# Performance work log

Hardware: AMD Instinct MI355X
Metric: run time of the kernel (lower is better)

## Reference

```python
import jax, jax.numpy as jnp
import numpy as np

POOL_SIZE = 100
TOP_K = 5
EPS = 1e-12

def l2_normalize(x, axis):
    # matches module: x * rsqrt(max(sum(x^2), eps))
    sq = jnp.sum(x * x, axis=axis, keepdims=True)
    return x * jax.lax.rsqrt(jnp.maximum(sq, EPS))

def setup_inputs() -> dict:
    key = jax.random.key(0)
    k1, k2 = jax.random.split(key)
    x_embed = jax.random.normal(k1, (256, 512, 768), dtype=jnp.float32)
    # prompt_key init 'uniform' -> U(-1, 1)
    prompt_key = jax.random.uniform(k2, (POOL_SIZE, 768), dtype=jnp.float32, minval=-1.0, maxval=1.0)
    return {"x_embed": x_embed, "prompt_key": prompt_key}

def reference(x_embed, prompt_key):
    B = x_embed.shape[0]
    # embedding_key == 'cls' with cls_features=None -> max over sequence dim
    x_embed_mean = jnp.max(x_embed, axis=1)                      # [B, D]
    prompt_norm = l2_normalize(prompt_key, axis=1)               # [P, D]
    x_embed_norm = l2_normalize(x_embed_mean, axis=1)            # [B, D]
    similarity = jnp.matmul(x_embed_norm, prompt_norm.T)         # [B, P]
    _, idx = jax.lax.top_k(similarity, TOP_K)                    # [B, K] (batchwise_prompt=False)
    selected_key = prompt_norm[idx]                              # [B, K, D] gather
    sim = selected_key * x_embed_norm[:, None, :]                # [B, K, D]
    reduce_sim = jnp.sum(sim) / B
    return similarity, selected_key, reduce_sim, idx
```

## Files before the change

kernel.cpp:

```cpp
#include <hip/hip_runtime.h>
#include <float.h>

#define B 256
#define S 512
#define D 768
#define P 100
#define K 5
#define SPLIT 4
#define SCHUNK (S / SPLIT)
#define D4 (D / 4)

#define PART_OFF 0
#define PN_OFF   (SPLIT * B * D)

#define SIM_OFF 0
#define SEL_OFF (B * P)
#define RS_OFF  (SEL_OFF + B * K * D)
#define IDX_OFF (RS_OFF + 1)

__device__ inline float4 fmax4(float4 a, float4 b) {
    return make_float4(fmaxf(a.x, b.x), fmaxf(a.y, b.y),
                       fmaxf(a.z, b.z), fmaxf(a.w, b.w));
}

__device__ inline float precise_rsqrt(float tot) {
    float x = fmaxf(tot, 1e-12f);
    float r = rsqrtf(x);
    r = r * (1.5f - 0.5f * x * r * r);
    return r;
}

__global__ __launch_bounds__(192) void k_stage1(const float* __restrict__ x,
                                                const float* __restrict__ pk,
                                                float* __restrict__ ws,
                                                float* __restrict__ out) {
    __shared__ float lds[3];
    const int blk = blockIdx.x;
    const int t = threadIdx.x;

    if (blk < B * SPLIT) {
        const int b  = blk >> 2;
        const int sp = blk & 3;
        const float4* src = (const float4*)(x + (size_t)b * S * D)
                            + (size_t)(sp * SCHUNK) * D4 + t;
        float4 m0 = make_float4(-FLT_MAX, -FLT_MAX, -FLT_MAX, -FLT_MAX);
        float4 m1 = m0, m2 = m0, m3 = m0;
        for (int s = 0; s < SCHUNK; s += 4) {
            float4 a0 = src[(size_t)(s + 0) * D4];
            float4 a1 = src[(size_t)(s + 1) * D4];
            float4 a2 = src[(size_t)(s + 2) * D4];
            float4 a3 = src[(size_t)(s + 3) * D4];
            m0 = fmax4(m0, a0);
            m1 = fmax4(m1, a1);
            m2 = fmax4(m2, a2);
            m3 = fmax4(m3, a3);
        }
        float4 m = fmax4(fmax4(m0, m1), fmax4(m2, m3));
        ((float4*)(ws + PART_OFF))[(size_t)(sp * B + b) * D4 + t] = m;
    } else {
        const int p = blk - B * SPLIT;
        float4 v = ((const float4*)pk)[(size_t)p * D4 + t];
        float sq = v.x * v.x + v.y * v.y + v.z * v.z + v.w * v.w;
        for (int off = 32; off; off >>= 1) sq += __shfl_down(sq, off);
        const int lane = t & 63, w = t >> 6;
        if (lane == 0) lds[w] = sq;
        __syncthreads();
        float tot = lds[0] + lds[1] + lds[2];
        float r = precise_rsqrt(tot);
        ((float4*)(ws + PN_OFF))[(size_t)p * D4 + t] =
            make_float4(v.x * r, v.y * r, v.z * r, v.w * r);
        if (p == 0 && t == 0) out[RS_OFF] = 0.0f;
    }
}

__global__ __launch_bounds__(256) void k_fused(const float* __restrict__ ws,
                                               float* __restrict__ out) {
    __shared__ float xs[D];
    __shared__ float simbuf[P];
    __shared__ float lds[4];
    __shared__ float topv[K];
    __shared__ int   topi[K];
    const int b = blockIdx.x, t = threadIdx.x;
    const int w = t >> 6, lane = t & 63;

    float4 m = make_float4(0.f, 0.f, 0.f, 0.f);
    float sq = 0.f;
    if (t < D4) {
        const float4* part = (const float4*)(ws + PART_OFF);
        m = part[(size_t)b * D4 + t];
        #pragma unroll
        for (int sp = 1; sp < SPLIT; ++sp)
            m = fmax4(m, part[(size_t)(sp * B + b) * D4 + t]);
        sq = m.x * m.x + m.y * m.y + m.z * m.z + m.w * m.w;
    }
    for (int off = 32; off; off >>= 1) sq += __shfl_down(sq, off);
    if (lane == 0) lds[w] = sq;
    __syncthreads();
    float tot = lds[0] + lds[1] + lds[2] + lds[3];
    float r = precise_rsqrt(tot);
    if (t < D4)
        ((float4*)xs)[t] = make_float4(m.x * r, m.y * r, m.z * r, m.w * r);
    __syncthreads();

    const float* pn = ws + PN_OFF;
    for (int j = 0; j < 25; ++j) {
        const int p = w + 4 * j;
        float acc = 0.f;
        #pragma unroll
        for (int jj = 0; jj < 12; ++jj) {
            const int d = lane + 64 * jj;
            acc += pn[(size_t)p * D + d] * xs[d];
        }
        for (int off = 32; off; off >>= 1) acc += __shfl_down(acc, off);
        if (lane == 0) {
            simbuf[p] = acc;
            out[SIM_OFF + (size_t)b * P + p] = acc;
        }
    }
    __syncthreads();

    if (w == 0) {
        float v0 = (lane < P) ? simbuf[lane] : -FLT_MAX;
        int   i0 = lane;
        int   i1 = lane + 64;
        float v1 = (i1 < P) ? simbuf[i1] : -FLT_MAX;
        for (int k = 0; k < K; ++k) {
            float bv; int bi;
            if (v0 > v1 || (v0 == v1 && i0 < i1)) { bv = v0; bi = i0; }
            else                                  { bv = v1; bi = i1; }
            for (int off = 32; off; off >>= 1) {
                float ov = __shfl_xor(bv, off);
                int   oi = __shfl_xor(bi, off);
                if (ov > bv || (ov == bv && oi < bi)) { bv = ov; bi = oi; }
            }
            if (lane == 0) { topv[k] = bv; topi[k] = bi; }
            if (bi == i0) v0 = -FLT_MAX;
            else if (bi == i1) v1 = -FLT_MAX;
        }
    }
    __syncthreads();

    if (t < K) out[IDX_OFF + (size_t)b * K + t] = (float)topi[t];

    if (t == 0) {
        float s = topv[0] + topv[1] + topv[2] + topv[3] + topv[4];
        atomicAdd(out + RS_OFF, s * (1.0f / (float)B));
    }

    const float4* pn4 = (const float4*)pn;
    float4* sel4 = (float4*)(out + SEL_OFF) + (size_t)b * (K * D4);
    for (int i = t; i < K * D4; i += 256) {
        const int k = i / D4;
        const int e = i - k * D4;
        sel4[i] = pn4[(size_t)topi[k] * D4 + e];
    }
}

extern "C" void kernel_launch(void* const* d_in, const int* in_sizes, int n_in,
                              void* d_out, int out_size, void* d_ws, size_t ws_size,
                              hipStream_t stream) {
    const float* x_embed    = (const float*)d_in[0];
    const float* prompt_key = (const float*)d_in[1];
    float* out = (float*)d_out;
    float* ws  = (float*)d_ws;

    k_stage1<<<B * SPLIT + P, 192, 0, stream>>>(x_embed, prompt_key, ws, out);
    k_fused<<<B, 256, 0, stream>>>(ws, out);
}
```

Before: 605.9 us.

## Fuse both kernels into one using last-block-done atomic counters

Merges the per-split max-reduction kernel and the per-batch similarity/top-k kernel into one launch. Per-batch atomic counters let the last finishing split block do the final reduction, similarity, top-k and gather, and it spin-waits on a counter until all prompt-normalization blocks are done. This removes a second kernel launch and the gap between the two kernels, but adds a memset launch, atomics and a spin-wait that depends on the prompt blocks being scheduled first. The tail work now runs with 192 threads instead of 256.

```diff
diff --git a/kernel.cpp b/kernel.cpp
--- a/kernel.cpp
+++ b/kernel.cpp
@@ -10,8 +10,8 @@
 #define SCHUNK (S / SPLIT)
 #define D4 (D / 4)
 
-#define PART_OFF 0
-#define PN_OFF   (SPLIT * B * D)
+#define PART_OFF 512
+#define PN_OFF   (PART_OFF + SPLIT * B * D)
 
 #define SIM_OFF 0
 #define SEL_OFF (B * P)
@@ -30,17 +30,44 @@
     return r;
 }
 
-__global__ __launch_bounds__(192) void k_stage1(const float* __restrict__ x,
-                                                const float* __restrict__ pk,
-                                                float* __restrict__ ws,
-                                                float* __restrict__ out) {
-    __shared__ float lds[3];
+__global__ __launch_bounds__(192) void k_all(const float* __restrict__ x,
+                                             const float* __restrict__ pk,
+                                             float* __restrict__ ws,
+                                             float* __restrict__ out) {
+    int* cnt     = (int*)ws;
+    int* pn_done = cnt + B;
     const int blk = blockIdx.x;
     const int t = threadIdx.x;
+    const int lane = t & 63, w = t >> 6;
 
-    if (blk < B * SPLIT) {
-        const int b  = blk >> 2;
-        const int sp = blk & 3;
+    __shared__ float lds[3];
+    __shared__ float xs[D];
+    __shared__ float simbuf[P];
+    __shared__ float topv[K];
+    __shared__ int   topi[K];
+    __shared__ int   is_last;
+
+    if (blk < P) {
+        const int p = blk;
+        float4 v = ((const float4*)pk)[(size_t)p * D4 + t];
+        float sq = v.x * v.x + v.y * v.y + v.z * v.z + v.w * v.w;
+        for (int off = 32; off; off >>= 1) sq += __shfl_down(sq, off);
+        if (lane == 0) lds[w] = sq;
+        __syncthreads();
+        float tot = lds[0] + lds[1] + lds[2];
+        float r = precise_rsqrt(tot);
+        ((float4*)(ws + PN_OFF))[(size_t)p * D4 + t] =
+            make_float4(v.x * r, v.y * r, v.z * r, v.w * r);
+        if (p == 0 && t == 0) out[RS_OFF] = 0.0f;
+        __syncthreads();
+        if (t == 0) { __threadfence(); atomicAdd(pn_done, 1); }
+        return;
+    }
+
+    const int bs = blk - P;
+    const int b  = bs >> 2;
+    const int sp = bs & 3;
+    {
         const float4* src = (const float4*)(x + (size_t)b * S * D)
                             + (size_t)(sp * SCHUNK) * D4 + t;
         float4 m0 = make_float4(-FLT_MAX, -FLT_MAX, -FLT_MAX, -FLT_MAX);
@@ -57,54 +84,42 @@
         }
         float4 m = fmax4(fmax4(m0, m1), fmax4(m2, m3));
         ((float4*)(ws + PART_OFF))[(size_t)(sp * B + b) * D4 + t] = m;
-    } else {
-        const int p = blk - B * SPLIT;
-        float4 v = ((const float4*)pk)[(size_t)p * D4 + t];
-        float sq = v.x * v.x + v.y * v.y + v.z * v.z + v.w * v.w;
-        for (int off = 32; off; off >>= 1) sq += __shfl_down(sq, off);
-        const int lane = t & 63, w = t >> 6;
-        if (lane == 0) lds[w] = sq;
-        __syncthreads();
-        float tot = lds[0] + lds[1] + lds[2];
-        float r = precise_rsqrt(tot);
-        ((float4*)(ws + PN_OFF))[(size_t)p * D4 + t] =
-            make_float4(v.x * r, v.y * r, v.z * r, v.w * r);
-        if (p == 0 && t == 0) out[RS_OFF] = 0.0f;
     }
-}
+    __syncthreads();
+    if (t == 0) {
+        __threadfence();
+        int old = atomicAdd(&cnt[b], 1);
+        is_last = (old == SPLIT - 1);
+    }
+    __syncthreads();
+    if (!is_last) return;
 
-__global__ __launch_bounds__(256) void k_fused(const float* __restrict__ ws,
-                                               float* __restrict__ out) {
-    __shared__ float xs[D];
-    __shared__ float simbuf[P];
-    __shared__ float lds[4];
-    __shared__ float topv[K];
-    __shared__ int   topi[K];
-    const int b = blockIdx.x, t = threadIdx.x;
-    const int w = t >> 6, lane = t & 63;
+    if (t == 0) {
+        while (__hip_atomic_load(pn_done, __ATOMIC_ACQUIRE,
+                                 __HIP_MEMORY_SCOPE_AGENT) < P)
+            __builtin_amdgcn_s_sleep(1);
+    }
+    __syncthreads();
+    __threadfence();
 
-    float4 m = make_float4(0.f, 0.f, 0.f, 0.f);
-    float sq = 0.f;
-    if (t < D4) {
-        const float4* part = (const float4*)(ws + PART_OFF);
-        m = part[(size_t)b * D4 + t];
-        #pragma unroll
-        for (int sp = 1; sp < SPLIT; ++sp)
-            m = fmax4(m, part[(size_t)(sp * B + b) * D4 + t]);
-        sq = m.x * m.x + m.y * m.y + m.z * m.z + m.w * m.w;
-    }
+    const float4* part = (const float4*)(ws + PART_OFF);
+    float4 m = part[(size_t)b * D4 + t];
+    #pragma unroll
+    for (int spp = 1; spp < SPLIT; ++spp)
+        m = fmax4(m, part[(size_t)(spp * B + b) * D4 + t]);
+    float sq = m.x * m.x + m.y * m.y + m.z * m.z + m.w * m.w;
     for (int off = 32; off; off >>= 1) sq += __shfl_down(sq, off);
     if (lane == 0) lds[w] = sq;
     __syncthreads();
-    float tot = lds[0] + lds[1] + lds[2] + lds[3];
+    float tot = lds[0] + lds[1] + lds[2];
     float r = precise_rsqrt(tot);
-    if (t < D4)
-        ((float4*)xs)[t] = make_float4(m.x * r, m.y * r, m.z * r, m.w * r);
+    ((float4*)xs)[t] = make_float4(m.x * r, m.y * r, m.z * r, m.w * r);
     __syncthreads();
 
     const float* pn = ws + PN_OFF;
-    for (int j = 0; j < 25; ++j) {
-        const int p = w + 4 * j;
+    for (int j = 0; j < 34; ++j) {
+        const int p = w + 3 * j;
+        if (p >= P) break;
         float acc = 0.f;
         #pragma unroll
         for (int jj = 0; jj < 12; ++jj) {
@@ -149,7 +164,7 @@
 
     const float4* pn4 = (const float4*)pn;
     float4* sel4 = (float4*)(out + SEL_OFF) + (size_t)b * (K * D4);
-    for (int i = t; i < K * D4; i += 256) {
+    for (int i = t; i < K * D4; i += 192) {
         const int k = i / D4;
         const int e = i - k * D4;
         sel4[i] = pn4[(size_t)topi[k] * D4 + e];
@@ -164,6 +179,6 @@
     float* out = (float*)d_out;
     float* ws  = (float*)d_ws;
 
-    k_stage1<<<B * SPLIT + P, 192, 0, stream>>>(x_embed, prompt_key, ws, out);
-    k_fused<<<B, 256, 0, stream>>>(ws, out);
+    hipMemsetAsync(ws, 0, (B + 1) * sizeof(int), stream);
+    k_all<<<P + B * SPLIT, 192, 0, stream>>>(x_embed, prompt_key, ws, out);
 }
```

New measurement: 690.0 us. +13.9%, slower.
